# Performance work log

Measured on AMD Instinct MI355X. Metric: run time of the kernel, lower is better.

Reference implementation:

```python
import jax, jax.numpy as jnp
import numpy as np

DIM = 1024
NH = 16        # query heads
NKV = 4        # kv heads
HD = 64        # head dim
GROUPS = NH // NKV
SPATIAL = 16
NZ = SPATIAL * SPATIAL  # 256 latent tokens with 2D structure
SOFT_CAP = 50.0
SCALE = HD ** -0.5
EPS = 1e-6


def rope_2d_cos_sin(nz, hd, spatial, dtype):
    # 2D RoPE: first half of head_dim encodes row position, second half column.
    pos = jnp.arange(nz)
    row = (pos // spatial).astype(jnp.float32)
    col = (pos % spatial).astype(jnp.float32)
    quarter = hd // 4
    inv_freq = 1.0 / (10000.0 ** (jnp.arange(quarter, dtype=jnp.float32) / quarter))
    f_row = row[:, None] * inv_freq[None, :]   # (nz, hd/4)
    f_col = col[:, None] * inv_freq[None, :]   # (nz, hd/4)
    emb = jnp.concatenate([f_row, f_col], axis=-1)      # (nz, hd/2)
    emb = jnp.concatenate([emb, emb], axis=-1)          # (nz, hd)
    return jnp.cos(emb).astype(dtype), jnp.sin(emb).astype(dtype)


def rotate_half(x):
    x1, x2 = jnp.split(x, 2, axis=-1)
    return jnp.concatenate([-x2, x1], axis=-1)


def apply_rotary(x, cos, sin):
    return x * cos + rotate_half(x) * sin


def rms_norm(x, w):
    # RMSNorm over head_dim with learned per-dim scale (QKNorm)
    return x * jax.lax.rsqrt(jnp.mean(x * x, axis=-1, keepdims=True) + EPS) * w


def setup_inputs() -> dict:
    key = jax.random.key(0)
    ks = jax.random.split(key, 7)
    B, T, S = 4, 16, 264
    x = jax.random.normal(ks[0], (B, T, S, DIM), dtype=jnp.float32)
    wq = jax.random.normal(ks[1], (NH * HD, DIM), dtype=jnp.float32) * 0.02
    wk = jax.random.normal(ks[2], (NKV * HD, DIM), dtype=jnp.float32) * 0.02
    wv = jax.random.normal(ks[3], (NKV * HD, DIM), dtype=jnp.float32) * 0.02
    wo = jax.random.normal(ks[4], (DIM, NH * HD), dtype=jnp.float32) * 0.02
    q_norm_w = jnp.ones((HD,), dtype=jnp.float32)
    k_norm_w = jnp.ones((HD,), dtype=jnp.float32)
    return {"x": x, "wq": wq, "wk": wk, "wv": wv, "wo": wo,
            "q_norm_w": q_norm_w, "k_norm_w": k_norm_w}


def reference(x, wq, wk, wv, wo, q_norm_w, k_norm_w):
    B, T, S, D = x.shape
    xf = x.reshape(B * T, S, D)
    # projections (torch Linear: y = x @ W.T)
    q = (xf @ wq.T).reshape(B * T, S, NH, HD).transpose(0, 2, 1, 3)   # (BT,NH,S,HD)
    k = (xf @ wk.T).reshape(B * T, S, NKV, HD).transpose(0, 2, 1, 3)  # (BT,NKV,S,HD)
    v = (xf @ wv.T).reshape(B * T, S, NKV, HD).transpose(0, 2, 1, 3)
    # QKNorm
    q = rms_norm(q, q_norm_w)
    k = rms_norm(k, k_norm_w)
    # partial 2D RoPE on latent tokens only
    cos, sin = rope_2d_cos_sin(NZ, HD, SPATIAL, q.dtype)
    cos = cos[None, None]  # (1,1,NZ,HD)
    sin = sin[None, None]
    q = jnp.concatenate([apply_rotary(q[:, :, :NZ], cos, sin), q[:, :, NZ:]], axis=2)
    k = jnp.concatenate([apply_rotary(k[:, :, :NZ], cos, sin), k[:, :, NZ:]], axis=2)
    # GQA: expand kv heads (repeat_interleave == jnp.repeat)
    k = jnp.repeat(k, GROUPS, axis=1)
    v = jnp.repeat(v, GROUPS, axis=1)
    # attention with soft cap
    attn = jnp.einsum("bhqd,bhkd->bhqk", q, k) * SCALE
    attn = SOFT_CAP * jnp.tanh(attn / SOFT_CAP)
    attn = jax.nn.softmax(attn, axis=-1)
    out = jnp.einsum("bhqk,bhkd->bhqd", attn, v)
    out = out.transpose(0, 2, 1, 3).reshape(B * T, S, NH * HD)
    out = out @ wo.T
    return out.reshape(B, T, S, D)
```

## Files before the change

### kernel.cpp

```cpp
#include <hip/hip_runtime.h>

typedef __bf16 bf16;
typedef __bf16 bf16x8 __attribute__((ext_vector_type(8)));
typedef float  f32x4  __attribute__((ext_vector_type(4)));

#define DIM   1024
#define NH    16
#define NKV   4
#define HD    64
#define SLEN  264
#define BTOT  64
#define MROWS (BTOT * SLEN)
#define NQKV  1536
#define NZ    256
#define VPAD  288

__device__ __forceinline__ void gl_lds16(const bf16* g, bf16* l) {
    __builtin_amdgcn_global_load_lds((__attribute__((address_space(1))) void*)(g),
                                     (__attribute__((address_space(3))) void*)(l),
                                     16, 0, 0);
}

__global__ void cvt_f32_bf16(const float* __restrict__ src, bf16* __restrict__ dst, int n) {
    int i = (blockIdx.x * 256 + threadIdx.x) * 4;
    if (i < n) {
        float4 v = *(const float4*)(src + i);
        dst[i + 0] = (bf16)v.x; dst[i + 1] = (bf16)v.y;
        dst[i + 2] = (bf16)v.z; dst[i + 3] = (bf16)v.w;
    }
}

__global__ void cvt_wcat(const float* __restrict__ wq, const float* __restrict__ wk,
                         const float* __restrict__ wv, bf16* __restrict__ dst) {
    int i = (blockIdx.x * 256 + threadIdx.x) * 4;
    const float* src; int off;
    if (i < 1024 * 1024)      { src = wq; off = i; }
    else if (i < 1280 * 1024) { src = wk; off = i - 1024 * 1024; }
    else                      { src = wv; off = i - 1280 * 1024; }
    float4 v = *(const float4*)(src + off);
    dst[i + 0] = (bf16)v.x; dst[i + 1] = (bf16)v.y;
    dst[i + 2] = (bf16)v.z; dst[i + 3] = (bf16)v.w;
}

__global__ void rope_tab_kernel(float2* __restrict__ ctab) {
    int i = blockIdx.x * 256 + threadIdx.x;
    int s = i >> 5, d = i & 31;
    const float LN1 = 0.5756462732485115f;
    float pos = (d < 16) ? (float)(s >> 4) : (float)(s & 15);
    float ang = pos * expf(-(float)(d & 15) * LN1);
    float sn, cs; sincosf(ang, &sn, &cs);
    ctab[i] = make_float2(cs, sn);
}

__global__ __launch_bounds__(256) void gemm_qkv(const bf16* __restrict__ A,
                                                const bf16* __restrict__ Bw,
                                                bf16* __restrict__ out,
                                                const float* __restrict__ qw,
                                                const float* __restrict__ kw,
                                                const float2* __restrict__ ctab) {
    __shared__ __align__(16) bf16 As[128 * 32];
    __shared__ __align__(16) bf16 Bs[128 * 32];
    const int tid  = threadIdx.x;
    const int wid  = tid >> 6, lane = tid & 63;
    const int quad = lane >> 4, r16 = lane & 15;
    const int bn = blockIdx.x, bm = blockIdx.y;
    const int wm = wid & 1, wn = wid >> 1;

    const bf16* Ag = A  + (size_t)(bm * 128 + (tid >> 2)) * DIM + (tid & 3) * 8;
    const bf16* Bg = Bw + (size_t)(bn * 128 + (tid >> 2)) * DIM + (tid & 3) * 8;
    bf16* AsW = As + wid * 512;
    bf16* BsW = Bs + wid * 512;

    f32x4 acc[4][4];
#pragma unroll
    for (int i = 0; i < 4; i++)
#pragma unroll
        for (int j = 0; j < 4; j++) acc[i][j] = (f32x4){0.f, 0.f, 0.f, 0.f};

    for (int k0 = 0; k0 < DIM; k0 += 32) {
        __syncthreads();
        gl_lds16(Ag + k0,             AsW);
        gl_lds16(Ag + 64 * DIM + k0,  AsW + 2048);
        gl_lds16(Bg + k0,             BsW);
        gl_lds16(Bg + 64 * DIM + k0,  BsW + 2048);
        __syncthreads();

        bf16x8 a[4], b[4];
#pragma unroll
        for (int i = 0; i < 4; i++) {
            a[i] = *(const bf16x8*)&As[(wm * 64 + i * 16 + r16) * 32 + quad * 8];
            b[i] = *(const bf16x8*)&Bs[(wn * 64 + i * 16 + r16) * 32 + quad * 8];
        }
#pragma unroll
        for (int i = 0; i < 4; i++)
#pragma unroll
            for (int j = 0; j < 4; j++)
                acc[i][j] = __builtin_amdgcn_mfma_f32_16x16x32_bf16(a[i], b[j], acc[i][j], 0, 0, 0);
    }

    const int colbase = bn * 128 + wn * 64;
    const int rowbase = bm * 128 + wm * 64;
    if (bn < 10) {
        const float* w = (bn < 8) ? qw : kw;
        float wreg[4];
#pragma unroll
        for (int j = 0; j < 4; j++) wreg[j] = w[j * 16 + r16];
#pragma unroll
        for (int i = 0; i < 4; i++)
#pragma unroll
            for (int r = 0; r < 4; r++) {
                float ss = 0.f;
#pragma unroll
                for (int j = 0; j < 4; j++) ss += acc[i][j][r] * acc[i][j][r];
                ss += __shfl_xor(ss, 1, 64);
                ss += __shfl_xor(ss, 2, 64);
                ss += __shfl_xor(ss, 4, 64);
                ss += __shfl_xor(ss, 8, 64);
                float rms = rsqrtf(ss * (1.f / 64.f) + 1e-6f);
                float xv[4];
#pragma unroll
                for (int j = 0; j < 4; j++) xv[j] = acc[i][j][r] * rms * wreg[j];
                int gm = rowbase + i * 16 + quad * 4 + r;
                int s = gm % SLEN;
                if (s < NZ) {
                    float2 cs0 = ctab[s * 32 + r16];
                    float2 cs1 = ctab[s * 32 + 16 + r16];
                    float a0 = xv[0] * cs0.x - xv[2] * cs0.y;
                    float a2 = xv[2] * cs0.x + xv[0] * cs0.y;
                    float a1 = xv[1] * cs1.x - xv[3] * cs1.y;
                    float a3 = xv[3] * cs1.x + xv[1] * cs1.y;
                    xv[0] = a0; xv[1] = a1; xv[2] = a2; xv[3] = a3;
                }
                size_t rowoff = (size_t)gm * NQKV + colbase + r16;
#pragma unroll
                for (int j = 0; j < 4; j++) out[rowoff + j * 16] = (bf16)xv[j];
            }
    } else {
#pragma unroll
        for (int i = 0; i < 4; i++)
#pragma unroll
            for (int j = 0; j < 4; j++)
#pragma unroll
                for (int r = 0; r < 4; r++) {
                    int gm = rowbase + i * 16 + quad * 4 + r;
                    int gn = colbase + j * 16 + r16;
                    out[(size_t)gm * NQKV + gn] = (bf16)acc[i][j][r];
                }
    }
}

__global__ __launch_bounds__(256) void gemm_bt(const bf16* __restrict__ A,
                                               const bf16* __restrict__ Bw,
                                               float* __restrict__ Cout,
                                               int Nld, int K) {
    __shared__ __align__(16) bf16 As[128 * 32];
    __shared__ __align__(16) bf16 Bs[128 * 32];
    const int tid  = threadIdx.x;
    const int wid  = tid >> 6, lane = tid & 63;
    const int quad = lane >> 4, r16 = lane & 15;
    const int bn = blockIdx.x, bm = blockIdx.y;
    const int wm = wid & 1, wn = wid >> 1;

    const bf16* Ag = A  + (size_t)(bm * 128 + (tid >> 2)) * K + (tid & 3) * 8;
    const bf16* Bg = Bw + (size_t)(bn * 128 + (tid >> 2)) * K + (tid & 3) * 8;
    bf16* AsW = As + wid * 512;
    bf16* BsW = Bs + wid * 512;

    f32x4 acc[4][4];
#pragma unroll
    for (int i = 0; i < 4; i++)
#pragma unroll
        for (int j = 0; j < 4; j++) acc[i][j] = (f32x4){0.f, 0.f, 0.f, 0.f};

    for (int k0 = 0; k0 < K; k0 += 32) {
        __syncthreads();
        gl_lds16(Ag + k0,           AsW);
        gl_lds16(Ag + 64 * K + k0,  AsW + 2048);
        gl_lds16(Bg + k0,           BsW);
        gl_lds16(Bg + 64 * K + k0,  BsW + 2048);
        __syncthreads();

        bf16x8 a[4], b[4];
#pragma unroll
        for (int i = 0; i < 4; i++) {
            a[i] = *(const bf16x8*)&As[(wm * 64 + i * 16 + r16) * 32 + quad * 8];
            b[i] = *(const bf16x8*)&Bs[(wn * 64 + i * 16 + r16) * 32 + quad * 8];
        }
#pragma unroll
        for (int i = 0; i < 4; i++)
#pragma unroll
            for (int j = 0; j < 4; j++)
                acc[i][j] = __builtin_amdgcn_mfma_f32_16x16x32_bf16(a[i], b[j], acc[i][j], 0, 0, 0);
    }

#pragma unroll
    for (int i = 0; i < 4; i++)
#pragma unroll
        for (int j = 0; j < 4; j++)
#pragma unroll
            for (int r = 0; r < 4; r++) {
                int gm = bm * 128 + wm * 64 + i * 16 + quad * 4 + r;
                int gn = bn * 128 + wn * 64 + j * 16 + r16;
                Cout[(size_t)gm * Nld + gn] = acc[i][j][r];
            }
}

__global__ __launch_bounds__(256) void vtrans_kernel(const bf16* __restrict__ qkv,
                                                     bf16* __restrict__ vt) {
    __shared__ bf16 Ls[64 * 272];
    const int tid = threadIdx.x;
    const int b = blockIdx.x, bt = b >> 2, kv = b & 3;
    const int part = tid >> 5;
    const int rr   = tid & 31;
#pragma unroll
    for (int pass = 0; pass < 9; ++pass) {
        int row = pass * 32 + rr;
        if (row < SLEN) {
            bf16x8 v = *(const bf16x8*)(qkv + (size_t)(bt * SLEN + row) * NQKV + 1280 + kv * 64 + part * 8);
#pragma unroll
            for (int j = 0; j < 8; j++) Ls[(part * 8 + j) * 272 + row] = v[j];
        }
    }
    __syncthreads();
    const int d = tid >> 2, seg = tid & 3;
    size_t obase = ((size_t)b * 64 + d) * VPAD;
#pragma unroll
    for (int m = 0; m < 9; ++m) {
        int col = seg * 72 + m * 8;
        bf16x8 o;
#pragma unroll
        for (int j = 0; j < 8; j++) {
            int s = col + j;
            o[j] = (s < SLEN) ? Ls[d * 272 + s] : (bf16)0.f;
        }
        *(bf16x8*)(vt + obase + col) = o;
    }
}

__global__ __launch_bounds__(256) void attn_kernel(const bf16* __restrict__ qkv,
                                                   const bf16* __restrict__ vt,
                                                   bf16* __restrict__ aout) {
    const int PLD = 40;
    __shared__ __align__(16) bf16 Pb[4][2][16 * PLD];

    const int tid = threadIdx.x;
    const int wid = tid >> 6, lane = tid & 63;
    const int quad = lane >> 4, r16 = lane & 15;
    const int qp = blockIdx.x;
    const int kv = blockIdx.y, bt = blockIdx.z;
    const int h = kv * 4 + wid;

    bf16x8 qa[2][2];
#pragma unroll
    for (int qi = 0; qi < 2; qi++) {
        int q0 = qp * 32 + qi * 16 + r16;
        int qcl = q0 < SLEN ? q0 : SLEN - 1;
        const bf16* qb = qkv + (size_t)(bt * SLEN + qcl) * NQKV + h * HD + quad * 8;
        qa[qi][0] = *(const bf16x8*)qb;
        qa[qi][1] = *(const bf16x8*)(qb + 32);
    }

    f32x4 oacc[2][4];
    float lsum[2][4];
#pragma unroll
    for (int qi = 0; qi < 2; qi++)
#pragma unroll
        for (int i = 0; i < 4; i++) { oacc[qi][i] = (f32x4){0.f, 0.f, 0.f, 0.f}; lsum[qi][i] = 0.f; }

    const bf16* kbase = qkv + (size_t)bt * SLEN * NQKV + 1024 + kv * HD + quad * 8;
    const bf16* vbase = vt + (size_t)(bt * 4 + kv) * HD * VPAD;

    bf16x8 nk[2][2];
#pragma unroll
    for (int kt = 0; kt < 2; kt++) {
        int key = kt * 16 + r16;
        const bf16* kp = kbase + (size_t)key * NQKV;
        nk[kt][0] = *(const bf16x8*)kp;
        nk[kt][1] = *(const bf16x8*)(kp + 32);
    }

    for (int c = 0; c < 9; ++c) {
        bf16x8 ck[2][2];
#pragma unroll
        for (int kt = 0; kt < 2; kt++) { ck[kt][0] = nk[kt][0]; ck[kt][1] = nk[kt][1]; }
        if (c < 8) {
#pragma unroll
            for (int kt = 0; kt < 2; kt++) {
                int key = (c + 1) * 32 + kt * 16 + r16;
                int kc = key < SLEN ? key : SLEN - 1;
                const bf16* kp = kbase + (size_t)kc * NQKV;
                nk[kt][0] = *(const bf16x8*)kp;
                nk[kt][1] = *(const bf16x8*)(kp + 32);
            }
        }
        bf16x8 cv[4];
#pragma unroll
        for (int dt = 0; dt < 4; ++dt)
            cv[dt] = *(const bf16x8*)(vbase + (size_t)(dt * 16 + r16) * VPAD + c * 32 + quad * 8);

        f32x4 s[2][2];
#pragma unroll
        for (int qi = 0; qi < 2; qi++)
#pragma unroll
            for (int kt = 0; kt < 2; kt++) {
                f32x4 t = (f32x4){0.f, 0.f, 0.f, 0.f};
                t = __builtin_amdgcn_mfma_f32_16x16x32_bf16(qa[qi][0], ck[kt][0], t, 0, 0, 0);
                t = __builtin_amdgcn_mfma_f32_16x16x32_bf16(qa[qi][1], ck[kt][1], t, 0, 0, 0);
                s[qi][kt] = t;
            }

#pragma unroll
        for (int qi = 0; qi < 2; qi++) {
            bf16* Pw = &Pb[wid][qi][0];
#pragma unroll
            for (int kt = 0; kt < 2; kt++)
#pragma unroll
                for (int r = 0; r < 4; ++r) {
                    int key = c * 32 + kt * 16 + r16;
                    float sc = s[qi][kt][r];
                    float z = sc * 0.0025f;
                    float z2 = z * z;
                    float poly = fmaf(z2, fmaf(z2, 0.133333333f, -0.333333333f), 1.f);
                    float p = exp2f(sc * 0.18033688f * poly);
                    p = (key < SLEN) ? p : 0.f;
                    bf16 pb = (bf16)p;
                    lsum[qi][r] += (float)pb;
                    Pw[(quad * 4 + r) * PLD + kt * 16 + r16] = pb;
                }
            bf16x8 pa = *(const bf16x8*)&Pw[r16 * PLD + quad * 8];
#pragma unroll
            for (int dt = 0; dt < 4; ++dt)
                oacc[qi][dt] = __builtin_amdgcn_mfma_f32_16x16x32_bf16(pa, cv[dt], oacc[qi][dt], 0, 0, 0);
        }
    }

#pragma unroll
    for (int qi = 0; qi < 2; qi++)
#pragma unroll
        for (int r = 0; r < 4; ++r) {
            float l = lsum[qi][r];
            l += __shfl_xor(l, 1, 64);
            l += __shfl_xor(l, 2, 64);
            l += __shfl_xor(l, 4, 64);
            l += __shfl_xor(l, 8, 64);
            float inv = 1.f / l;
            int q = qp * 32 + qi * 16 + quad * 4 + r;
            if (q < SLEN) {
                size_t base = (size_t)(bt * SLEN + q) * (NH * HD) + h * HD;
#pragma unroll
                for (int dt = 0; dt < 4; ++dt)
                    aout[base + dt * 16 + r16] = (bf16)(oacc[qi][dt][r] * inv);
            }
        }
}

extern "C" void kernel_launch(void* const* d_in, const int* in_sizes, int n_in,
                              void* d_out, int out_size, void* d_ws, size_t ws_size,
                              hipStream_t stream) {
    const float* x   = (const float*)d_in[0];
    const float* wq  = (const float*)d_in[1];
    const float* wk  = (const float*)d_in[2];
    const float* wv  = (const float*)d_in[3];
    const float* wo  = (const float*)d_in[4];
    const float* qnw = (const float*)d_in[5];
    const float* knw = (const float*)d_in[6];

    bf16* xbf  = (bf16*)d_ws;
    bf16* wcat = xbf  + (size_t)MROWS * DIM;
    bf16* wobf = wcat + (size_t)NQKV * DIM;
    bf16* qkv  = wobf + (size_t)DIM * DIM;
    bf16* vt   = qkv  + (size_t)MROWS * NQKV;
    float2* ctab = (float2*)(vt + (size_t)BTOT * NKV * HD * VPAD);
    bf16* aout = xbf;

    rope_tab_kernel<<<32, 256, 0, stream>>>(ctab);
    cvt_f32_bf16<<<(MROWS * DIM) / 1024, 256, 0, stream>>>(x, xbf, MROWS * DIM);
    cvt_wcat<<<(NQKV * DIM) / 1024, 256, 0, stream>>>(wq, wk, wv, wcat);
    cvt_f32_bf16<<<(DIM * DIM) / 1024, 256, 0, stream>>>(wo, wobf, DIM * DIM);

    gemm_qkv<<<dim3(NQKV / 128, MROWS / 128), 256, 0, stream>>>(xbf, wcat, qkv, qnw, knw, ctab);
    vtrans_kernel<<<BTOT * NKV, 256, 0, stream>>>(qkv, vt);
    attn_kernel<<<dim3(9, NKV, BTOT), 256, 0, stream>>>(qkv, vt, aout);
    gemm_bt<<<dim3(DIM / 128, MROWS / 128), 256, 0, stream>>>(aout, wobf, (float*)d_out, DIM, DIM);
}
```

Before: 385.9 us.

## Deepen GEMM K-tile to 64 with XOR-swizzled LDS and grouped block rasterization

Both bf16 GEMMs (QKV projection and output projection) now stage a 128x64 K-slice per iteration instead of 128x32. This halves the number of barrier pairs and doubles the MFMA work done between syncs. LDS rows are XOR-swizzled by row to avoid bank conflicts when fragments are read at the wider row stride. Blocks are launched on a 1D grid remapped so that groups of 4 M-tiles sweep across N, which improves L2 reuse of the A tiles; the cost is doubled LDS per block, which may lower occupancy.

Measured after the change: 355.5 us. 1.09x faster.

```diff
diff --git a/kernel.cpp b/kernel.cpp
--- a/kernel.cpp
+++ b/kernel.cpp
@@ -52,24 +52,40 @@
     ctab[i] = make_float2(cs, sn);
 }
 
+#define GEMM_STAGE_PTRS(Mptr, tileRow, K, P)                                   \
+    const bf16* P[4];                                                          \
+    {                                                                          \
+        _Pragma("unroll")                                                      \
+        for (int k = 0; k < 4; k++) {                                          \
+            int s = k * 256 + tid;                                             \
+            int r = s >> 3, cp = s & 7;                                        \
+            int c = cp ^ (r & 7);                                              \
+            P[k] = (Mptr) + (size_t)((tileRow) + r) * (K) + c * 8;             \
+        }                                                                      \
+    }
+
+__device__ __forceinline__ int swz(int row, int chunk) {
+    return row * 64 + ((chunk ^ (row & 7)) * 8);
+}
+
 __global__ __launch_bounds__(256) void gemm_qkv(const bf16* __restrict__ A,
                                                 const bf16* __restrict__ Bw,
                                                 bf16* __restrict__ out,
                                                 const float* __restrict__ qw,
                                                 const float* __restrict__ kw,
                                                 const float2* __restrict__ ctab) {
-    __shared__ __align__(16) bf16 As[128 * 32];
-    __shared__ __align__(16) bf16 Bs[128 * 32];
+    __shared__ __align__(16) bf16 As[128 * 64];
+    __shared__ __align__(16) bf16 Bs[128 * 64];
     const int tid  = threadIdx.x;
     const int wid  = tid >> 6, lane = tid & 63;
     const int quad = lane >> 4, r16 = lane & 15;
-    const int bn = blockIdx.x, bm = blockIdx.y;
+    const int bid = blockIdx.x;
+    const int g = bid / 48, rr = bid - g * 48;
+    const int bm = g * 4 + (rr & 3), bn = rr >> 2;
     const int wm = wid & 1, wn = wid >> 1;
 
-    const bf16* Ag = A  + (size_t)(bm * 128 + (tid >> 2)) * DIM + (tid & 3) * 8;
-    const bf16* Bg = Bw + (size_t)(bn * 128 + (tid >> 2)) * DIM + (tid & 3) * 8;
-    bf16* AsW = As + wid * 512;
-    bf16* BsW = Bs + wid * 512;
+    GEMM_STAGE_PTRS(A,  bm * 128, DIM, Ap)
+    GEMM_STAGE_PTRS(Bw, bn * 128, DIM, Bp)
 
     f32x4 acc[4][4];
 #pragma unroll
@@ -77,25 +93,28 @@
 #pragma unroll
         for (int j = 0; j < 4; j++) acc[i][j] = (f32x4){0.f, 0.f, 0.f, 0.f};
 
-    for (int k0 = 0; k0 < DIM; k0 += 32) {
+    for (int k0 = 0; k0 < DIM; k0 += 64) {
         __syncthreads();
-        gl_lds16(Ag + k0,             AsW);
-        gl_lds16(Ag + 64 * DIM + k0,  AsW + 2048);
-        gl_lds16(Bg + k0,             BsW);
-        gl_lds16(Bg + 64 * DIM + k0,  BsW + 2048);
+#pragma unroll
+        for (int k = 0; k < 4; k++) {
+            gl_lds16(Ap[k] + k0, As + (k * 256 + wid * 64) * 8);
+            gl_lds16(Bp[k] + k0, Bs + (k * 256 + wid * 64) * 8);
+        }
         __syncthreads();
-
-        bf16x8 a[4], b[4];
-#pragma unroll
-        for (int i = 0; i < 4; i++) {
-            a[i] = *(const bf16x8*)&As[(wm * 64 + i * 16 + r16) * 32 + quad * 8];
-            b[i] = *(const bf16x8*)&Bs[(wn * 64 + i * 16 + r16) * 32 + quad * 8];
-        }
-#pragma unroll
-        for (int i = 0; i < 4; i++)
-#pragma unroll
-            for (int j = 0; j < 4; j++)
-                acc[i][j] = __builtin_amdgcn_mfma_f32_16x16x32_bf16(a[i], b[j], acc[i][j], 0, 0, 0);
+#pragma unroll
+        for (int ks = 0; ks < 2; ks++) {
+            bf16x8 a[4], b[4];
+#pragma unroll
+            for (int i = 0; i < 4; i++) {
+                a[i] = *(const bf16x8*)&As[swz(wm * 64 + i * 16 + r16, ks * 4 + quad)];
+                b[i] = *(const bf16x8*)&Bs[swz(wn * 64 + i * 16 + r16, ks * 4 + quad)];
+            }
+#pragma unroll
+            for (int i = 0; i < 4; i++)
+#pragma unroll
+                for (int j = 0; j < 4; j++)
+                    acc[i][j] = __builtin_amdgcn_mfma_f32_16x16x32_bf16(a[i], b[j], acc[i][j], 0, 0, 0);
+        }
     }
 
     const int colbase = bn * 128 + wn * 64;
@@ -151,20 +170,19 @@
 
 __global__ __launch_bounds__(256) void gemm_bt(const bf16* __restrict__ A,
                                                const bf16* __restrict__ Bw,
-                                               float* __restrict__ Cout,
-                                               int Nld, int K) {
-    __shared__ __align__(16) bf16 As[128 * 32];
-    __shared__ __align__(16) bf16 Bs[128 * 32];
+                                               float* __restrict__ Cout) {
+    __shared__ __align__(16) bf16 As[128 * 64];
+    __shared__ __align__(16) bf16 Bs[128 * 64];
     const int tid  = threadIdx.x;
     const int wid  = tid >> 6, lane = tid & 63;
     const int quad = lane >> 4, r16 = lane & 15;
-    const int bn = blockIdx.x, bm = blockIdx.y;
+    const int bid = blockIdx.x;
+    const int g = bid / 32, rr = bid - g * 32;
+    const int bm = g * 4 + (rr & 3), bn = rr >> 2;
     const int wm = wid & 1, wn = wid >> 1;
 
-    const bf16* Ag = A  + (size_t)(bm * 128 + (tid >> 2)) * K + (tid & 3) * 8;
-    const bf16* Bg = Bw + (size_t)(bn * 128 + (tid >> 2)) * K + (tid & 3) * 8;
-    bf16* AsW = As + wid * 512;
-    bf16* BsW = Bs + wid * 512;
+    GEMM_STAGE_PTRS(A,  bm * 128, DIM, Ap)
+    GEMM_STAGE_PTRS(Bw, bn * 128, DIM, Bp)
 
     f32x4 acc[4][4];
 #pragma unroll
@@ -172,25 +190,28 @@
 #pragma unroll
         for (int j = 0; j < 4; j++) acc[i][j] = (f32x4){0.f, 0.f, 0.f, 0.f};
 
-    for (int k0 = 0; k0 < K; k0 += 32) {
+    for (int k0 = 0; k0 < DIM; k0 += 64) {
         __syncthreads();
-        gl_lds16(Ag + k0,           AsW);
-        gl_lds16(Ag + 64 * K + k0,  AsW + 2048);
-        gl_lds16(Bg + k0,           BsW);
-        gl_lds16(Bg + 64 * K + k0,  BsW + 2048);
+#pragma unroll
+        for (int k = 0; k < 4; k++) {
+            gl_lds16(Ap[k] + k0, As + (k * 256 + wid * 64) * 8);
+            gl_lds16(Bp[k] + k0, Bs + (k * 256 + wid * 64) * 8);
+        }
         __syncthreads();
-
-        bf16x8 a[4], b[4];
-#pragma unroll
-        for (int i = 0; i < 4; i++) {
-            a[i] = *(const bf16x8*)&As[(wm * 64 + i * 16 + r16) * 32 + quad * 8];
-            b[i] = *(const bf16x8*)&Bs[(wn * 64 + i * 16 + r16) * 32 + quad * 8];
-        }
-#pragma unroll
-        for (int i = 0; i < 4; i++)
-#pragma unroll
-            for (int j = 0; j < 4; j++)
-                acc[i][j] = __builtin_amdgcn_mfma_f32_16x16x32_bf16(a[i], b[j], acc[i][j], 0, 0, 0);
+#pragma unroll
+        for (int ks = 0; ks < 2; ks++) {
+            bf16x8 a[4], b[4];
+#pragma unroll
+            for (int i = 0; i < 4; i++) {
+                a[i] = *(const bf16x8*)&As[swz(wm * 64 + i * 16 + r16, ks * 4 + quad)];
+                b[i] = *(const bf16x8*)&Bs[swz(wn * 64 + i * 16 + r16, ks * 4 + quad)];
+            }
+#pragma unroll
+            for (int i = 0; i < 4; i++)
+#pragma unroll
+                for (int j = 0; j < 4; j++)
+                    acc[i][j] = __builtin_amdgcn_mfma_f32_16x16x32_bf16(a[i], b[j], acc[i][j], 0, 0, 0);
+        }
     }
 
 #pragma unroll
@@ -201,7 +222,7 @@
             for (int r = 0; r < 4; r++) {
                 int gm = bm * 128 + wm * 64 + i * 16 + quad * 4 + r;
                 int gn = bn * 128 + wn * 64 + j * 16 + r16;
-                Cout[(size_t)gm * Nld + gn] = acc[i][j][r];
+                Cout[(size_t)gm * DIM + gn] = acc[i][j][r];
             }
 }
 
@@ -378,8 +399,8 @@
     cvt_wcat<<<(NQKV * DIM) / 1024, 256, 0, stream>>>(wq, wk, wv, wcat);
     cvt_f32_bf16<<<(DIM * DIM) / 1024, 256, 0, stream>>>(wo, wobf, DIM * DIM);
 
-    gemm_qkv<<<dim3(NQKV / 128, MROWS / 128), 256, 0, stream>>>(xbf, wcat, qkv, qnw, knw, ctab);
+    gemm_qkv<<<(MROWS / 128) * (NQKV / 128), 256, 0, stream>>>(xbf, wcat, qkv, qnw, knw, ctab);
     vtrans_kernel<<<BTOT * NKV, 256, 0, stream>>>(qkv, vt);
     attn_kernel<<<dim3(9, NKV, BTOT), 256, 0, stream>>>(qkv, vt, aout);
-    gemm_bt<<<dim3(DIM / 128, MROWS / 128), 256, 0, stream>>>(aout, wobf, (float*)d_out, DIM, DIM);
-}
+    gemm_bt<<<(MROWS / 128) * (DIM / 128), 256, 0, stream>>>(aout, wobf, (float*)d_out);
+}
```
